# Kernel tuning notes

Hardware: AMD Instinct MI355X
Metric: run time of the kernel (lower is better)

## Reference

```python
import jax, jax.numpy as jnp
import numpy as np

B, L, ENC, DEC, HID = 256, 196, 2048, 512, 512


def setup_inputs() -> dict:
    key = jax.random.key(0)
    ks = jax.random.split(key, 8)
    s_enc = 1.0 / np.sqrt(ENC)
    s_dec = 1.0 / np.sqrt(DEC)
    s_hid = 1.0 / np.sqrt(HID)
    return {
        "feature": jax.random.normal(ks[0], (B, L, ENC), dtype=jnp.float32),
        "hidden": jax.random.normal(ks[1], (B, DEC), dtype=jnp.float32),
        # nn.Linear params (PyTorch default uniform init ranges)
        "Wf": jax.random.uniform(ks[2], (HID, ENC), jnp.float32, -s_enc, s_enc),
        "bf": jax.random.uniform(ks[3], (HID,), jnp.float32, -s_enc, s_enc),
        "Wh": jax.random.uniform(ks[4], (HID, DEC), jnp.float32, -s_dec, s_dec),
        "bh": jax.random.uniform(ks[5], (HID,), jnp.float32, -s_dec, s_dec),
        "We": jax.random.uniform(ks[6], (1, HID), jnp.float32, -s_hid, s_hid),
        "be": jax.random.uniform(ks[7], (1,), jnp.float32, -s_hid, s_hid),
    }


def reference(feature, hidden, Wf, bf, Wh, bh, We, be):
    # feature: [B, L, ENC], hidden: [B, DEC]
    feat_emb = jnp.einsum("ble,he->blh", feature, Wf) + bf          # [B, L, HID]
    hid_emb = (hidden @ Wh.T + bh)[:, None, :]                        # [B, 1, HID]
    emb = jax.nn.relu(feat_emb + hid_emb)                             # [B, L, HID]
    score = jnp.einsum("blh,h->bl", emb, We[0]) + be[0]               # [B, L]
    weight = jax.nn.softmax(score, axis=1)                            # [B, L]
    output = jnp.einsum("bl,ble->be", weight, feature)                # [B, ENC]
    return (output, weight)
```

## Files before the change

### kernel.cpp

```cpp
#include <hip/hip_runtime.h>
#include <hip/hip_bf16.h>
#include <math.h>

#define B_   256
#define L_   196
#define ENC_ 2048
#define DEC_ 512
#define HID_ 512

typedef __attribute__((ext_vector_type(8))) short short8v;
typedef __attribute__((ext_vector_type(4))) short short4v;
typedef __attribute__((ext_vector_type(4))) float f32x4;

static __device__ __forceinline__ short f2bf(float x) {
    unsigned u = __float_as_uint(x);
    u += 0x7fffu + ((u >> 16) & 1u);
    return (short)(u >> 16);
}

__global__ __launch_bounds__(256) void kconvert(const float* __restrict__ Wf,
                                                short* __restrict__ wfbf) {
    int idx = (blockIdx.x * 256 + threadIdx.x) * 4;
    int n  = idx >> 11;
    int e0 = idx & 2047;
    float4 f = *(const float4*)(Wf + idx);
    short4v h;
    h.x = f2bf(f.x); h.y = f2bf(f.y); h.z = f2bf(f.z); h.w = f2bf(f.w);
    int tile = e0 >> 5;
    int lu   = (e0 >> 3) & 3;
    int pu   = lu ^ ((n >> 1) & 3);
    int off  = n * 2048 + tile * 32 + pu * 8 + (e0 & 7);
    *(short4v*)(wfbf + off) = h;
}

__global__ __launch_bounds__(512) void khid(const float* __restrict__ hidden,
                                            const float* __restrict__ Wh,
                                            const float* __restrict__ bh,
                                            float* __restrict__ hid_emb) {
    __shared__ float hs[8][512];
    int t = threadIdx.x;
    int bg = blockIdx.x * 8;
    #pragma unroll
    for (int i = 0; i < 8; ++i) hs[i][t] = hidden[(size_t)(bg + i) * 512 + t];
    __syncthreads();
    float acc[8] = {0.f,0.f,0.f,0.f,0.f,0.f,0.f,0.f};
    const float4* wrow = (const float4*)(Wh + (size_t)t * 512);
    #pragma unroll 4
    for (int d4 = 0; d4 < 128; ++d4) {
        float4 w = wrow[d4];
        int d = d4 * 4;
        #pragma unroll
        for (int i = 0; i < 8; ++i)
            acc[i] += w.x * hs[i][d] + w.y * hs[i][d+1] + w.z * hs[i][d+2] + w.w * hs[i][d+3];
    }
    float bhv = bh[t];
    #pragma unroll
    for (int i = 0; i < 8; ++i)
        hid_emb[(size_t)(bg + i) * 512 + t] = acc[i] + bhv;
}

__global__ __launch_bounds__(512, 4) void kscore(
    const float* __restrict__ feat, const short* __restrict__ wfbf,
    const float* __restrict__ bf, const float* __restrict__ hid_emb,
    const float* __restrict__ We, const float* __restrict__ be,
    float* __restrict__ score)
{
    __shared__ short lds_b[2 * 512 * 32];
    __shared__ short lds_a[2 * 64 * 32];
    __shared__ float score_s[8][64];

    const int tid  = threadIdx.x;
    const int wave = tid >> 6;
    const int lane = tid & 63;
    const int g    = lane >> 4;
    const int c    = lane & 15;
    const int m0   = blockIdx.x * 64;

    const int r_a  = tid >> 3;
    const int c4   = tid & 7;
    const float* gA = feat + (size_t)(m0 + r_a) * ENC_ + c4 * 4;
    const int boffA = r_a * 64 + (((c4 >> 1) ^ ((r_a >> 1) & 3)) << 4) + (c4 & 1) * 8;

    f32x4 acc[4][4];
    #pragma unroll
    for (int i = 0; i < 4; ++i)
        #pragma unroll
        for (int j = 0; j < 4; ++j)
            acc[i][j] = (f32x4)0.f;

#define STAGE_B(K0, BUF)                                                      \
    {                                                                         \
        short* bbase = lds_b + (size_t)(BUF) * 16384;                         \
        _Pragma("unroll")                                                     \
        for (int j = 0; j < 4; ++j) {                                         \
            int ubase = j * 512 + wave * 64;       \
            int ulin  = ubase + lane;              \
            int n = ulin >> 2, u = ulin & 3;                                  \
            const short* gp = wfbf + (size_t)n * ENC_ + (K0) + u * 8;         \
            short* lp = bbase + (size_t)ubase * 8;                            \
            __builtin_amdgcn_global_load_lds(                                 \
                (const __attribute__((address_space(1))) void*)gp,            \
                (__attribute__((address_space(3))) void*)lp, 16, 0, 0);       \
        }                                                                     \
    }

#define COMPUTE_TILE(BUF)                                                     \
    {                                                                         \
        const char* la = (const char*)lds_a + (BUF) * 4096;                   \
        const char* lb = (const char*)lds_b + (BUF) * 32768;                  \
        short8v af[4], bq[4];                                                 \
        _Pragma("unroll")                                                     \
        for (int mi = 0; mi < 4; ++mi) {                                      \
            int row = mi * 16 + c;                                            \
            int un  = g ^ ((row >> 1) & 3);                                   \
            af[mi] = *(const short8v*)(la + row * 64 + un * 16);              \
        }                                                                     \
        _Pragma("unroll")                                                     \
        for (int ni = 0; ni < 4; ++ni) {                                      \
            int n  = wave * 64 + ni * 16 + c;                                 \
            int un = g ^ ((n >> 1) & 3);                                      \
            bq[ni] = *(const short8v*)(lb + n * 64 + un * 16);                \
        }                                                                     \
        _Pragma("unroll")                                                     \
        for (int mi = 0; mi < 4; ++mi)                                        \
            _Pragma("unroll")                                                 \
            for (int ni = 0; ni < 4; ++ni)                                    \
                acc[mi][ni] = __builtin_amdgcn_mfma_f32_16x16x32_bf16(        \
                    af[mi], bq[ni], acc[mi][ni], 0, 0, 0);                    \
    }

#define WRITE_A(FA, BUF)                                                      \
    {                                                                         \
        short4v h0;                                                           \
        h0.x = f2bf((FA).x); h0.y = f2bf((FA).y);                             \
        h0.z = f2bf((FA).z); h0.w = f2bf((FA).w);                             \
        char* wa = (char*)lds_a + (BUF) * 4096;                               \
        *(short4v*)(wa + boffA) = h0;                                         \
    }

#define BAR_COUNTED(N)                                                        \
    asm volatile("s_waitcnt vmcnt(" #N ") lgkmcnt(0)" ::: "memory");          \
    __builtin_amdgcn_sched_barrier(0);                                        \
    __builtin_amdgcn_s_barrier();                                             \
    __builtin_amdgcn_sched_barrier(0);

    float4 fa_cur = *(const float4*)(gA);
    STAGE_B(0, 0)
    float4 fa_nxt = *(const float4*)(gA + 32);
    WRITE_A(fa_cur, 0)
    fa_cur = fa_nxt;
    BAR_COUNTED(1)

    for (int kt = 0; kt < 62; ++kt) {
        const int pcur = kt & 1;
        STAGE_B((kt + 1) * 32, pcur ^ 1)
        fa_nxt = *(const float4*)(gA + (kt + 2) * 32);
        COMPUTE_TILE(pcur)
        WRITE_A(fa_cur, pcur ^ 1)
        fa_cur = fa_nxt;
        BAR_COUNTED(1)
    }
    STAGE_B(63 * 32, 1)
    COMPUTE_TILE(0)
    WRITE_A(fa_cur, 1)
    BAR_COUNTED(0)
    COMPUTE_TILE(1)

#undef STAGE_B
#undef COMPUTE_TILE
#undef WRITE_A
#undef BAR_COUNTED

    float wev[4], bfv[4];
    #pragma unroll
    for (int ni = 0; ni < 4; ++ni) {
        int n = wave * 64 + ni * 16 + c;
        wev[ni] = We[n];
        bfv[ni] = bf[n];
    }
    #pragma unroll
    for (int mi = 0; mi < 4; ++mi) {
        float part[4] = {0.f, 0.f, 0.f, 0.f};
        #pragma unroll
        for (int j = 0; j < 4; ++j) {
            int row  = mi * 16 + g * 4 + j;
            int bidx = (m0 + row) / 196;
            const float* hrow = hid_emb + (size_t)bidx * 512;
            #pragma unroll
            for (int ni = 0; ni < 4; ++ni) {
                int n = wave * 64 + ni * 16 + c;
                float v = acc[mi][ni][j] + bfv[ni] + hrow[n];
                v = fmaxf(v, 0.f);
                part[j] += v * wev[ni];
            }
        }
        #pragma unroll
        for (int j = 0; j < 4; ++j) {
            float p = part[j];
            p += __shfl_xor(p, 1, 16);
            p += __shfl_xor(p, 2, 16);
            p += __shfl_xor(p, 4, 16);
            p += __shfl_xor(p, 8, 16);
            if (c == 0) score_s[wave][mi * 16 + g * 4 + j] = p;
        }
    }
    __syncthreads();
    if (tid < 64) {
        float s = be[0];
        #pragma unroll
        for (int w = 0; w < 8; ++w) s += score_s[w][tid];
        score[m0 + tid] = s;
    }
}

__global__ __launch_bounds__(256) void kout(
    const float* __restrict__ score, const float* __restrict__ feat,
    float* __restrict__ out_o, float* __restrict__ out_w)
{
    __shared__ float wbuf[196];
    __shared__ float red[8];
    int t    = threadIdx.x;
    int b    = blockIdx.x >> 1;
    int half = blockIdx.x & 1;
    int w    = t >> 6, lane = t & 63;

    float s = (t < 196) ? score[b * 196 + t] : -1e30f;
    float m = s;
    #pragma unroll
    for (int off = 32; off >= 1; off >>= 1) m = fmaxf(m, __shfl_xor(m, off, 64));
    if (lane == 0) red[w] = m;
    __syncthreads();
    m = fmaxf(fmaxf(red[0], red[1]), fmaxf(red[2], red[3]));
    float e = (t < 196) ? __expf(s - m) : 0.f;
    float sum = e;
    #pragma unroll
    for (int off = 32; off >= 1; off >>= 1) sum += __shfl_xor(sum, off, 64);
    if (lane == 0) red[4 + w] = sum;
    __syncthreads();
    sum = red[4] + red[5] + red[6] + red[7];
    float wt = e / sum;
    if (t < 196) {
        wbuf[t] = wt;
        if (half == 0) out_w[b * 196 + t] = wt;
    }
    __syncthreads();

    int e0 = half * 1024 + t * 4;
    float4 acc = make_float4(0.f, 0.f, 0.f, 0.f);
    const float* fb = feat + (size_t)b * L_ * ENC_ + e0;
    #pragma unroll 4
    for (int l = 0; l < 196; ++l) {
        float4 v = *(const float4*)(fb + (size_t)l * ENC_);
        float wl = wbuf[l];
        acc.x += wl * v.x; acc.y += wl * v.y; acc.z += wl * v.z; acc.w += wl * v.w;
    }
    *(float4*)(out_o + (size_t)b * ENC_ + e0) = acc;
}

extern "C" void kernel_launch(void* const* d_in, const int* in_sizes, int n_in,
                              void* d_out, int out_size, void* d_ws, size_t ws_size,
                              hipStream_t stream) {
    (void)in_sizes; (void)n_in; (void)out_size; (void)ws_size;
    const float* feature = (const float*)d_in[0];
    const float* hidden  = (const float*)d_in[1];
    const float* Wf      = (const float*)d_in[2];
    const float* bf      = (const float*)d_in[3];
    const float* Wh      = (const float*)d_in[4];
    const float* bh      = (const float*)d_in[5];
    const float* We      = (const float*)d_in[6];
    const float* be      = (const float*)d_in[7];

    char* ws = (char*)d_ws;
    short* wfbf    = (short*)ws;
    float* hid_emb = (float*)(ws + (2u << 20));
    float* score   = (float*)(ws + (2u << 20) + (512u << 10));

    float* out_o = (float*)d_out;
    float* out_w = out_o + (size_t)B_ * ENC_;

    kconvert<<<dim3(1024), dim3(256), 0, stream>>>(Wf, wfbf);
    khid<<<dim3(32), dim3(512), 0, stream>>>(hidden, Wh, bh, hid_emb);
    kscore<<<dim3(784), dim3(512), 0, stream>>>(feature, wfbf, bf, hid_emb, We, be, score);
    kout<<<dim3(512), dim3(256), 0, stream>>>(score, feature, (float*)d_out, out_w);
}
```

Before: 318.8 us.

## Split GEMM k-loop into two phases interleaving LDS reads, loads and MFMA

Restructures the main GEMM loop into a ping-pong schedule. Each k-tile is split into two MFMA halves separated by block barriers, and the second half's B-fragment reads and the A-tile LDS write are interleaved between them. MFMA sections are wrapped in s_setprio to favour matrix issue across waves. The aim is to overlap LDS traffic and global loads with MFMA work, at the cost of extra barriers per iteration.

Result: slower. 342.7 us (+7.5%).

```diff
diff --git a/kernel.cpp b/kernel.cpp
--- a/kernel.cpp
+++ b/kernel.cpp
@@ -93,8 +93,8 @@
         short* bbase = lds_b + (size_t)(BUF) * 16384;                         \
         _Pragma("unroll")                                                     \
         for (int j = 0; j < 4; ++j) {                                         \
-            int ubase = j * 512 + wave * 64;       \
-            int ulin  = ubase + lane;              \
+            int ubase = j * 512 + wave * 64;           \
+            int ulin  = ubase + lane;                  \
             int n = ulin >> 2, u = ulin & 3;                                  \
             const short* gp = wfbf + (size_t)n * ENC_ + (K0) + u * 8;         \
             short* lp = bbase + (size_t)ubase * 8;                            \
@@ -104,30 +104,38 @@
         }                                                                     \
     }
 
-#define COMPUTE_TILE(BUF)                                                     \
+#define RD_AF(BUF)                                                            \
     {                                                                         \
         const char* la = (const char*)lds_a + (BUF) * 4096;                   \
-        const char* lb = (const char*)lds_b + (BUF) * 32768;                  \
-        short8v af[4], bq[4];                                                 \
         _Pragma("unroll")                                                     \
         for (int mi = 0; mi < 4; ++mi) {                                      \
             int row = mi * 16 + c;                                            \
             int un  = g ^ ((row >> 1) & 3);                                   \
             af[mi] = *(const short8v*)(la + row * 64 + un * 16);              \
         }                                                                     \
+    }
+
+#define RD_BQ(BUF, N0, D0)                                                    \
+    {                                                                         \
+        const char* lb = (const char*)lds_b + (size_t)(BUF) * 32768;          \
         _Pragma("unroll")                                                     \
-        for (int ni = 0; ni < 4; ++ni) {                                      \
-            int n  = wave * 64 + ni * 16 + c;                                 \
+        for (int q = 0; q < 2; ++q) {                                         \
+            int n  = wave * 64 + ((N0) + q) * 16 + c;                         \
             int un = g ^ ((n >> 1) & 3);                                      \
-            bq[ni] = *(const short8v*)(lb + n * 64 + un * 16);                \
+            bq[(D0) + q] = *(const short8v*)(lb + n * 64 + un * 16);          \
         }                                                                     \
-        _Pragma("unroll")                                                     \
-        for (int mi = 0; mi < 4; ++mi)                                        \
-            _Pragma("unroll")                                                 \
-            for (int ni = 0; ni < 4; ++ni)                                    \
-                acc[mi][ni] = __builtin_amdgcn_mfma_f32_16x16x32_bf16(        \
-                    af[mi], bq[ni], acc[mi][ni], 0, 0, 0);                    \
-    }
+    }
+
+#define MFMA_HALF(B0, Q0)                                                     \
+    __builtin_amdgcn_s_setprio(1);                                            \
+    _Pragma("unroll")                                                         \
+    for (int mi = 0; mi < 4; ++mi) {                                          \
+        acc[mi][(B0)]   = __builtin_amdgcn_mfma_f32_16x16x32_bf16(            \
+            af[mi], bq[(Q0)],   acc[mi][(B0)],   0, 0, 0);                    \
+        acc[mi][(B0)+1] = __builtin_amdgcn_mfma_f32_16x16x32_bf16(            \
+            af[mi], bq[(Q0)+1], acc[mi][(B0)+1], 0, 0, 0);                    \
+    }                                                                         \
+    __builtin_amdgcn_s_setprio(0);
 
 #define WRITE_A(FA, BUF)                                                      \
     {                                                                         \
@@ -138,39 +146,69 @@
         *(short4v*)(wa + boffA) = h0;                                         \
     }
 
-#define BAR_COUNTED(N)                                                        \
-    asm volatile("s_waitcnt vmcnt(" #N ") lgkmcnt(0)" ::: "memory");          \
+#define SBAR                                                                  \
     __builtin_amdgcn_sched_barrier(0);                                        \
     __builtin_amdgcn_s_barrier();                                             \
     __builtin_amdgcn_sched_barrier(0);
 
+#define LGKM0                                                                 \
+    asm volatile("s_waitcnt lgkmcnt(0)" ::: "memory");                        \
+    __builtin_amdgcn_sched_barrier(0);
+
+#define VM1_LGKM0                                                             \
+    asm volatile("s_waitcnt vmcnt(1) lgkmcnt(0)" ::: "memory");               \
+    __builtin_amdgcn_sched_barrier(0);
+
+    short8v af[4], bq[4];
+
+    STAGE_B(0, 0)
     float4 fa_cur = *(const float4*)(gA);
-    STAGE_B(0, 0)
     float4 fa_nxt = *(const float4*)(gA + 32);
     WRITE_A(fa_cur, 0)
     fa_cur = fa_nxt;
-    BAR_COUNTED(1)
-
-    for (int kt = 0; kt < 62; ++kt) {
-        const int pcur = kt & 1;
-        STAGE_B((kt + 1) * 32, pcur ^ 1)
-        fa_nxt = *(const float4*)(gA + (kt + 2) * 32);
-        COMPUTE_TILE(pcur)
-        WRITE_A(fa_cur, pcur ^ 1)
+    asm volatile("s_waitcnt lgkmcnt(0)" ::: "memory");
+    SBAR
+
+    for (int kt = 0; kt < 63; ++kt) {
+        const int buf = kt & 1;
+        RD_AF(buf)
+        RD_BQ(buf, 0, 0)
+        STAGE_B((kt + 1) * 32, buf ^ 1)
+        {
+            const int ka = (kt + 2 > 63) ? 63 : kt + 2;
+            fa_nxt = *(const float4*)(gA + ka * 32);
+        }
+        SBAR
+        LGKM0
+        MFMA_HALF(0, 0)
+        SBAR
+        RD_BQ(buf, 2, 2)
+        WRITE_A(fa_cur, buf ^ 1)
         fa_cur = fa_nxt;
-        BAR_COUNTED(1)
-    }
-    STAGE_B(63 * 32, 1)
-    COMPUTE_TILE(0)
-    WRITE_A(fa_cur, 1)
-    BAR_COUNTED(0)
-    COMPUTE_TILE(1)
+        SBAR
+        LGKM0
+        MFMA_HALF(2, 2)
+        VM1_LGKM0
+        SBAR
+    }
+    RD_AF(1)
+    RD_BQ(1, 0, 0)
+    LGKM0
+    MFMA_HALF(0, 0)
+    RD_BQ(1, 2, 2)
+    LGKM0
+    MFMA_HALF(2, 2)
 
 #undef STAGE_B
-#undef COMPUTE_TILE
+#undef RD_AF
+#undef RD_BQ
+#undef MFMA_HALF
 #undef WRITE_A
-#undef BAR_COUNTED
-
+#undef SBAR
+#undef LGKM0
+#undef VM1_LGKM0
+
+    __syncthreads();
     float wev[4], bfv[4];
     #pragma unroll
     for (int ni = 0; ni < 4; ++ni) {
```
